# Kernel optimization log

Measured on AMD Instinct MI355X. Metric: run time of the kernel, lower is better.

## Reference

```python
import jax, jax.numpy as jnp
import numpy as np

# --- tkbn KbNufftAdjoint defaults for im_size=(128,128) ---
H, W = 128, 128          # im_size
GX, GY = 256, 256        # grid_size = 2 * im_size (default oversampling)
J = 6                    # numpoints (KB kernel width)
ALPHA = 2.34 * J         # tkbn default kb_alpha
I0_ALPHA = float(np.i0(ALPHA))


def _kb_ft_1d(om):
    # Fourier transform of order-0 Kaiser-Bessel kernel (Fessler), d=1.
    z = np.sqrt((np.pi * J * om) ** 2 - ALPHA ** 2 + 0j)
    return np.real(J * np.sinc(z / np.pi)) / np.i0(ALPHA)


def _apodization():
    # scaling coefficients: 1 / FT(kb) at centered image coords (tkbn compute_scaling_coefs)
    ax = 1.0 / _kb_ft_1d((np.arange(H) - (H - 1) / 2.0) / GX)
    ay = 1.0 / _kb_ft_1d((np.arange(W) - (W - 1) / 2.0) / GY)
    return jnp.asarray(np.outer(ax, ay), dtype=jnp.float32)  # [H, W]


def _kb_weights(gm, G):
    # gm: [K] fractional grid coords. Returns weights [K, J] and wrapped indices [K, J].
    base = jnp.floor(gm - J / 2.0)                       # [K]
    k = base[:, None] + jnp.arange(1, J + 1)[None, :]    # [K, J], offsets in (-J/2, J/2]
    u = gm[:, None] - k
    arg = 1.0 - (2.0 * u / J) ** 2
    w = jnp.where(arg > 0, jnp.i0(ALPHA * jnp.sqrt(jnp.maximum(arg, 1e-12))) / I0_ALPHA, 0.0)
    return w.astype(jnp.float32), jnp.mod(k, G).astype(jnp.int32)


def setup_inputs() -> dict:
    key = jax.random.key(0)
    k1, k2 = jax.random.split(key)
    values = jax.random.normal(k1, (8, 4, 32768), dtype=jnp.float32)
    coords = (jax.random.uniform(k2, (32768, 2), dtype=jnp.float32) * 2.0 - 1.0) * jnp.pi
    return {"values": values, "coords": coords}


def reference(values, coords):
    B, C, K = values.shape
    apod = _apodization()  # [H, W]

    # --- KB adjoint interpolation (gridding) onto oversampled grid ---
    gm_x = coords[:, 0] * (GX / (2.0 * jnp.pi))  # [K] fractional grid coords
    gm_y = coords[:, 1] * (GY / (2.0 * jnp.pi))
    wx, kx = _kb_weights(gm_x, GX)               # [K, J]
    wy, ky = _kb_weights(gm_y, GY)
    w = (wx[:, :, None] * wy[:, None, :]).reshape(K, J * J)                 # [K, 36]
    idx = (kx[:, :, None] * GY + ky[:, None, :]).reshape(K * J * J)        # [K*36]

    vals = values.astype(jnp.complex64)
    contrib = (vals[:, :, :, None] * w[None, None]).reshape(B, C, K * J * J)
    grid = jnp.zeros((B, C, GX * GY), dtype=jnp.complex64).at[:, :, idx].add(contrib)
    grid = grid.reshape(B, C, GX, GY)

    # --- true adjoint of unnormalized FFT: N * ifft, crop, apodize ---
    img = jnp.fft.ifft2(grid) * (GX * GY)
    img = img[..., :H, :W] * apod[None, None]    # [B, C, H, W] complex64

    # --- recon = |fftshift(fft2(img))| ; torch fftshift shifts ALL dims by default ---
    recon = jnp.abs(jnp.fft.fftshift(jnp.fft.fft2(img)))
    return recon
```

## Files before the change

### kernel.cpp

```cpp
#include <hip/hip_runtime.h>
#include <math.h>

#define NPTS 32768
#define CAPP 192
#define CAPC 57
#define SCALE ((float)(256.0 / (2.0 * M_PI)))

typedef __attribute__((ext_vector_type(8))) short short8b;
typedef __attribute__((ext_vector_type(4))) float f32x4;

static __device__ __forceinline__ unsigned short f2bf(float x) {
    unsigned u = __float_as_uint(x);
    return (unsigned short)((u + 0x7fffu + ((u >> 16) & 1u)) >> 16);
}

static __device__ __forceinline__ float bessel_i0f(float x) {
    float hx2 = 0.25f * x * x;
    float t = 1.0f, s = 1.0f;
#pragma unroll
    for (int m = 1; m <= 30; ++m) { t *= hx2 * (1.0f / ((float)m * (float)m)); s += t; }
    return s;
}

__global__ void k_zero(unsigned* __restrict__ tc) {
    tc[blockIdx.x * 256 + threadIdx.x] = 0u;
}

__global__ __launch_bounds__(256) void k_front(
        const float* __restrict__ coords, const float* __restrict__ values,
        unsigned short* __restrict__ Sfrag, float* __restrict__ wxy,
        unsigned* __restrict__ tileCount, unsigned* __restrict__ bins,
        float* __restrict__ vt) {
    __shared__ float tile[32][257];
    __shared__ float axf[128];
    __shared__ float2 sSh[256];
    int blk = blockIdx.x;
    int t = threadIdx.x;

    if (blk < 128) {
        int k = blk * 256 + t;
        const float inv_i0a = 1.0f / bessel_i0f(14.04f);
        float2 cv = *(const float2*)&coords[2 * k];
        float gmx = cv.x * SCALE;
        float gmy = cv.y * SCALE;
        float bxf = floorf(gmx - 3.0f), byf = floorf(gmy - 3.0f);
        float wl[12];
#pragma unroll
        for (int j = 0; j < 6; ++j) {
            float ux = gmx - (bxf + (float)(j + 1));
            float rx = ux * (1.0f / 3.0f);
            float argx = 1.0f - rx * rx;
            wl[j] = (argx > 0.0f) ? bessel_i0f(14.04f * sqrtf(argx)) * inv_i0a : 0.0f;
            float uy = gmy - (byf + (float)(j + 1));
            float ry = uy * (1.0f / 3.0f);
            float argy = 1.0f - ry * ry;
            wl[6 + j] = (argy > 0.0f) ? bessel_i0f(14.04f * sqrtf(argy)) * inv_i0a : 0.0f;
        }
        float4* wp = (float4*)&wxy[k * 12];
        wp[0] = *(const float4*)&wl[0];
        wp[1] = *(const float4*)&wl[4];
        wp[2] = *(const float4*)&wl[8];
        int x0 = (((int)bxf) + 1 + 512) & 255;
        int y0 = (((int)byf) + 1 + 512) & 255;
        int tx0 = x0 >> 3, tx1 = ((x0 + 5) & 255) >> 3;
        int ty0 = y0 >> 3, ty1 = ((y0 + 5) & 255) >> 3;
        int nx = (tx1 == tx0) ? 1 : 2;
        int ny = (ty1 == ty0) ? 1 : 2;
        int txs[2] = {tx0, tx1}, tys[2] = {ty0, ty1};
        for (int i = 0; i < nx; ++i)
            for (int j = 0; j < ny; ++j) {
                int tl = txs[i] * 32 + tys[j];
                unsigned ex = (unsigned)((x0 - 8 * txs[i] + 256) & 255);
                unsigned ey = (unsigned)((y0 - 8 * tys[j] + 256) & 255);
                unsigned pos = atomicAdd(&tileCount[tl * 16], 1u);
                if (pos < CAPP) bins[tl * CAPP + pos] = ((unsigned)k << 16) | (ex << 8) | ey;
            }
    } else {
        int kbase = (blk - 128) * 256;
        for (int img = 0; img < 32; ++img)
            tile[img][t] = values[img * NPTS + kbase + t];
        __syncthreads();
        int img = t & 31;
        int k0 = t >> 5;
        for (int r = 0; r < 32; ++r) {
            int kl = k0 + r * 8;
            vt[(kbase + kl) * 32 + img] = tile[img][kl];
        }
        int s = blk - 128;
        if (s < 8) {
            if (t < 128) {
                const float inv_i0a = 1.0f / bessel_i0f(14.04f);
                float om = ((float)t - 63.5f) * (1.0f / 256.0f);
                float pj = (float)M_PI * 6.0f * om;
                float tt = sqrtf(14.04f * 14.04f - pj * pj);
                float kbft = 6.0f * (sinhf(tt) / tt) * inv_i0a;
                axf[t] = 1.0f / kbft;
            }
            __syncthreads();
            float sw, cw;
            __sincosf((float)t * (float)(2.0 * M_PI / 256.0), &sw, &cw);
            float zr = 1.0f, zi = 0.0f, re = 0.0f, im = 0.0f;
            for (int x = 0; x < 128; ++x) {
                float a = axf[x];
                re = fmaf(a, zr, re);
                im = fmaf(a, zi, im);
                float nzr = zr * cw - zi * sw;
                zi = fmaf(zr, sw, zi * cw);
                zr = nzr;
            }
            sSh[t] = make_float2(re, im);
            __syncthreads();
            for (int idx = s * 4096 + t; idx < (s + 1) * 4096; idx += 256) {
                int i   = idx & 7;
                int ln  = (idx >> 3) & 63;
                int ks  = (idx >> 9) & 7;
                int tl  = idx >> 12;
                int si = (32 * ks + 8 * (ln >> 4) + i - 2 * (16 * tl + (ln & 15))) & 255;
                float2 sv = sSh[si];
                Sfrag[idx]         = f2bf(sv.x);
                Sfrag[32768 + idx] = f2bf(sv.y);
                Sfrag[65536 + idx] = f2bf(-sv.y);
            }
        }
    }
}

__global__ __launch_bounds__(256) void k_gather_tile(
        const float* __restrict__ wxy, const float* __restrict__ vt,
        const unsigned* __restrict__ tileCount, const unsigned* __restrict__ bins,
        unsigned short* __restrict__ Gt) {
    __shared__ unsigned cnt[64];
    __shared__ unsigned lists[64 * CAPC];
    __shared__ unsigned bsh[CAPP];
    __shared__ unsigned short gsh[64][40];
    int tile = blockIdx.x;
    int TX = tile >> 5, TY = tile & 31;
    int t = threadIdx.x;
    if (t < 64) cnt[t] = 0u;
    unsigned n = tileCount[tile * 16];
    if (n > CAPP) n = CAPP;
    for (int p = t; p < (int)n; p += 256) bsh[p] = bins[tile * CAPP + p];
    __syncthreads();
    int total = (int)n * 6;
    for (int task = t; task < total; task += 256) {
        int pi = task / 6;
        int jx = task - pi * 6;
        unsigned en = bsh[pi];
        int ex = (int)((en >> 8) & 255u);
        int ey = (int)(en & 255u);
        if (((ex + jx) & 255) < 8) {
            unsigned k = en >> 16;
            float wxv = wxy[k * 12 + jx];
            int lx = ((ex + jx) & 7) << 3;
            unsigned kq = k << 16;
            int jy0, jy1;
            if (ey <= 7) { jy0 = 0; jy1 = (7 - ey < 5) ? 7 - ey : 5; }
            else         { jy0 = 256 - ey; jy1 = 5; }
            for (int jy = jy0; jy <= jy1; ++jy) {
                float w = wxv * wxy[k * 12 + 6 + jy];
                unsigned q = (unsigned)(w * 65535.0f + 0.5f);
                if (q > 65535u) q = 65535u;
                int cl = lx | ((ey + jy) & 7);
                unsigned pos = atomicAdd(&cnt[cl], 1u);
                if (pos < CAPC) lists[cl * CAPC + pos] = kq | q;
            }
        }
    }
    __syncthreads();
    int c = t >> 2;
    int ib = (t & 3) * 8;
    unsigned nc = cnt[c];
    if (nc > CAPC) nc = CAPC;
    float acc0 = 0, acc1 = 0, acc2 = 0, acc3 = 0, acc4 = 0, acc5 = 0, acc6 = 0, acc7 = 0;
    for (unsigned e = 0; e < nc; ++e) {
        unsigned en = lists[c * CAPC + e];
        float w = (float)(en & 0xFFFFu) * (1.0f / 65535.0f);
        const float* vp = &vt[(en >> 16) * 32 + ib];
        float4 va = *(const float4*)vp;
        float4 vb = *(const float4*)(vp + 4);
        acc0 += w * va.x; acc1 += w * va.y; acc2 += w * va.z; acc3 += w * va.w;
        acc4 += w * vb.x; acc5 += w * vb.y; acc6 += w * vb.z; acc7 += w * vb.w;
    }
    {
        unsigned short* gp = &gsh[c][ib];
        gp[0] = f2bf(acc0); gp[1] = f2bf(acc1); gp[2] = f2bf(acc2); gp[3] = f2bf(acc3);
        gp[4] = f2bf(acc4); gp[5] = f2bf(acc5); gp[6] = f2bf(acc6); gp[7] = f2bf(acc7);
    }
    __syncthreads();
    {
        int img = t >> 3;
        int vr = t & 7;
        short8b row;
#pragma unroll
        for (int uu = 0; uu < 8; ++uu)
            row[uu] = (short)gsh[(uu << 3) | vr][img];
        *(short8b*)&Gt[img * 65536 + (((TY << 3) + vr) << 8) + (TX << 3)] = row;
    }
}

__global__ __launch_bounds__(512) void k_mmx(const unsigned short* __restrict__ Gt,
                                             const unsigned short* __restrict__ Sfrag,
                                             float* __restrict__ out) {
    __shared__ unsigned short T1[2][16][264];
    int t = threadIdx.x;
    int lane = t & 63;
    int w = t >> 6;
    int band = blockIdx.x;
    int img = blockIdx.y;
    int g4 = lane >> 4;
    int l15 = lane & 15;

    {
        int var = w >> 2;
        const unsigned short* sf = Sfrag + var * 32768 + band * 4096 + lane * 8;
        short8b a[8];
#pragma unroll
        for (int ks = 0; ks < 8; ++ks)
            a[ks] = *(const short8b*)(sf + ks * 512);
        const unsigned short* gimg = Gt + img * 65536 + 8 * g4;
#pragma unroll
        for (int j = 0; j < 4; ++j) {
            int vtile = (w & 3) + j * 4;
            int v0 = vtile * 16;
            const unsigned short* gb = gimg + (v0 + l15) * 256;
            f32x4 acc = {0.f, 0.f, 0.f, 0.f};
#pragma unroll
            for (int ks = 0; ks < 8; ++ks) {
                short8b b = *(const short8b*)(gb + ks * 32);
                acc = __builtin_amdgcn_mfma_f32_16x16x32_bf16(a[ks], b, acc, 0, 0, 0);
            }
            int vcol = v0 + l15;
#pragma unroll
            for (int r = 0; r < 4; ++r) {
                int p = g4 * 4 + r;
                T1[var][p][vcol ^ ((p & 7) << 3)] = f2bf(acc[r]);
            }
        }
    }
    __syncthreads();

    {
        int qt = w;
        const unsigned short* sfq = Sfrag + qt * 4096 + lane * 8;
        int swz = (l15 & 7) << 3;
        f32x4 accR = {0.f, 0.f, 0.f, 0.f}, accI = {0.f, 0.f, 0.f, 0.f};
#pragma unroll
        for (int ks = 0; ks < 8; ++ks) {
            int vidx = (32 * ks + 8 * g4) ^ swz;
            short8b aR = *(const short8b*)&T1[0][l15][vidx];
            short8b aI = *(const short8b*)&T1[1][l15][vidx];
            short8b bR = *(const short8b*)(sfq + ks * 512);
            short8b bI = *(const short8b*)(sfq + 32768 + ks * 512);
            short8b bN = *(const short8b*)(sfq + 65536 + ks * 512);
            accR = __builtin_amdgcn_mfma_f32_16x16x32_bf16(aR, bR, accR, 0, 0, 0);
            accR = __builtin_amdgcn_mfma_f32_16x16x32_bf16(aI, bN, accR, 0, 0, 0);
            accI = __builtin_amdgcn_mfma_f32_16x16x32_bf16(aR, bI, accI, 0, 0, 0);
            accI = __builtin_amdgcn_mfma_f32_16x16x32_bf16(aI, bR, accI, 0, 0, 0);
        }
        int q = qt * 16 + l15;
        int b_ = img >> 2, c_ = img & 3;
        int obase = ((b_ ^ 4) * 4 + (c_ ^ 2)) * 128;
#pragma unroll
        for (int r = 0; r < 4; ++r) {
            int p = band * 16 + g4 * 4 + r;
            float re = accR[r], im = accI[r];
            out[((obase + (p ^ 64)) << 7) + (q ^ 64)] = sqrtf(re * re + im * im);
        }
    }
}

extern "C" void kernel_launch(void* const* d_in, const int* in_sizes, int n_in,
                              void* d_out, int out_size, void* d_ws, size_t ws_size,
                              hipStream_t stream) {
    const float* values = (const float*)d_in[0];
    const float* coords = (const float*)d_in[1];

    char* ws = (char*)d_ws;
    unsigned short* Sfrag = (unsigned short*)(ws + 0);
    unsigned* tileCount   = (unsigned*)(ws + 196608);
    float*    wxy         = (float*)(ws + 262144);
    unsigned* bins        = (unsigned*)(ws + 1835008);
    unsigned short* Gt    = (unsigned short*)(ws + 2621440);
    float*    vt          = (float*)(ws + 6815744);

    k_zero<<<64, 256, 0, stream>>>(tileCount);
    k_front<<<256, 256, 0, stream>>>(coords, values, Sfrag, wxy, tileCount, bins, vt);
    k_gather_tile<<<1024, 256, 0, stream>>>(wxy, vt, tileCount, bins, Gt);
    k_mmx<<<dim3(8, 32), 512, 0, stream>>>(Gt, Sfrag, (float*)d_out);
}
```

Measured before the change: 50.43 us.

## Fuse all four kernels into one cooperative persistent kernel with grid syncs

Replaces the zero, front, gather and mmx launches with a single cooperative kernel of 256 blocks × 512 threads, separated by grid-wide syncs. Each block now handles four gather tiles, two per 256-thread half, using a shared-memory union. The aim is to remove three kernel launch gaps and the tail drain between stages. In exchange it adds grid-sync overhead and lowers parallelism in the gather stage, with 256 blocks instead of 1024.

```diff
diff --git a/kernel.cpp b/kernel.cpp
--- a/kernel.cpp
+++ b/kernel.cpp
@@ -1,5 +1,8 @@
 #include <hip/hip_runtime.h>
+#include <hip/hip_cooperative_groups.h>
 #include <math.h>
+
+namespace cg = cooperative_groups;
 
 #define NPTS 32768
 #define CAPP 192
@@ -22,23 +25,25 @@
     return s;
 }
 
-__global__ void k_zero(unsigned* __restrict__ tc) {
-    tc[blockIdx.x * 256 + threadIdx.x] = 0u;
-}
-
-__global__ __launch_bounds__(256) void k_front(
+__global__ __launch_bounds__(512) void k_mega(
         const float* __restrict__ coords, const float* __restrict__ values,
         unsigned short* __restrict__ Sfrag, float* __restrict__ wxy,
         unsigned* __restrict__ tileCount, unsigned* __restrict__ bins,
-        float* __restrict__ vt) {
-    __shared__ float tile[32][257];
-    __shared__ float axf[128];
-    __shared__ float2 sSh[256];
+        float* __restrict__ vt, unsigned short* __restrict__ Gt,
+        float* __restrict__ out) {
+    __shared__ __align__(16) char smem[41984];
+    cg::grid_group grid = cg::this_grid();
     int blk = blockIdx.x;
     int t = threadIdx.x;
 
-    if (blk < 128) {
-        int k = blk * 256 + t;
+    {
+        int gid = blk * 512 + t;
+        if (gid < 16384) tileCount[gid] = 0u;
+    }
+    grid.sync();
+
+    if (blk < 64) {
+        int k = blk * 512 + t;
         const float inv_i0a = 1.0f / bessel_i0f(14.04f);
         float2 cv = *(const float2*)&coords[2 * k];
         float gmx = cv.x * SCALE;
@@ -75,28 +80,32 @@
                 unsigned pos = atomicAdd(&tileCount[tl * 16], 1u);
                 if (pos < CAPP) bins[tl * CAPP + pos] = ((unsigned)k << 16) | (ex << 8) | ey;
             }
-    } else {
-        int kbase = (blk - 128) * 256;
-        for (int img = 0; img < 32; ++img)
-            tile[img][t] = values[img * NPTS + kbase + t];
+    } else if (blk < 192) {
+        float (*tile)[257] = (float(*)[257])smem;
+        int kbase = (blk - 64) * 256;
+        int col = t & 255;
+        for (int img = t >> 8; img < 32; img += 2)
+            tile[img][col] = values[img * NPTS + kbase + col];
         __syncthreads();
         int img = t & 31;
         int k0 = t >> 5;
-        for (int r = 0; r < 32; ++r) {
-            int kl = k0 + r * 8;
+        for (int r = 0; r < 16; ++r) {
+            int kl = k0 + r * 16;
             vt[(kbase + kl) * 32 + img] = tile[img][kl];
         }
-        int s = blk - 128;
-        if (s < 8) {
-            if (t < 128) {
-                const float inv_i0a = 1.0f / bessel_i0f(14.04f);
-                float om = ((float)t - 63.5f) * (1.0f / 256.0f);
-                float pj = (float)M_PI * 6.0f * om;
-                float tt = sqrtf(14.04f * 14.04f - pj * pj);
-                float kbft = 6.0f * (sinhf(tt) / tt) * inv_i0a;
-                axf[t] = 1.0f / kbft;
-            }
-            __syncthreads();
+    } else if (blk < 200) {
+        float* axf = (float*)smem;
+        float2* sSh = (float2*)(smem + 512);
+        if (t < 128) {
+            const float inv_i0a = 1.0f / bessel_i0f(14.04f);
+            float om = ((float)t - 63.5f) * (1.0f / 256.0f);
+            float pj = (float)M_PI * 6.0f * om;
+            float tt = sqrtf(14.04f * 14.04f - pj * pj);
+            float kbft = 6.0f * (sinhf(tt) / tt) * inv_i0a;
+            axf[t] = 1.0f / kbft;
+        }
+        __syncthreads();
+        if (t < 256) {
             float sw, cw;
             __sincosf((float)t * (float)(2.0 * M_PI / 256.0), &sw, &cw);
             float zr = 1.0f, zi = 0.0f, re = 0.0f, im = 0.0f;
@@ -109,162 +118,164 @@
                 zr = nzr;
             }
             sSh[t] = make_float2(re, im);
+        }
+        __syncthreads();
+        int s = blk - 192;
+        for (int idx = s * 4096 + t; idx < (s + 1) * 4096; idx += 512) {
+            int i   = idx & 7;
+            int ln  = (idx >> 3) & 63;
+            int ks  = (idx >> 9) & 7;
+            int tl  = idx >> 12;
+            int si = (32 * ks + 8 * (ln >> 4) + i - 2 * (16 * tl + (ln & 15))) & 255;
+            float2 sv = sSh[si];
+            Sfrag[idx]         = f2bf(sv.x);
+            Sfrag[32768 + idx] = f2bf(sv.y);
+            Sfrag[65536 + idx] = f2bf(-sv.y);
+        }
+    }
+    grid.sync();
+
+    {
+        int s = t >> 8;
+        int tt = t & 255;
+        char* base = smem + s * 20736;
+        unsigned* cnt = (unsigned*)base;
+        unsigned* lists = cnt + 64;
+        unsigned* bsh = lists + 64 * CAPC;
+        unsigned short (*gsh)[40] = (unsigned short(*)[40])(bsh + CAPP);
+        for (int ti = 0; ti < 2; ++ti) {
+            int tile = blk * 4 + s * 2 + ti;
+            int TX = tile >> 5, TY = tile & 31;
             __syncthreads();
-            for (int idx = s * 4096 + t; idx < (s + 1) * 4096; idx += 256) {
-                int i   = idx & 7;
-                int ln  = (idx >> 3) & 63;
-                int ks  = (idx >> 9) & 7;
-                int tl  = idx >> 12;
-                int si = (32 * ks + 8 * (ln >> 4) + i - 2 * (16 * tl + (ln & 15))) & 255;
-                float2 sv = sSh[si];
-                Sfrag[idx]         = f2bf(sv.x);
-                Sfrag[32768 + idx] = f2bf(sv.y);
-                Sfrag[65536 + idx] = f2bf(-sv.y);
+            if (tt < 64) cnt[tt] = 0u;
+            unsigned n = tileCount[tile * 16];
+            if (n > CAPP) n = CAPP;
+            for (int p = tt; p < (int)n; p += 256) bsh[p] = bins[tile * CAPP + p];
+            __syncthreads();
+            int total = (int)n * 6;
+            for (int task = tt; task < total; task += 256) {
+                int pi = task / 6;
+                int jx = task - pi * 6;
+                unsigned en = bsh[pi];
+                int ex = (int)((en >> 8) & 255u);
+                int ey = (int)(en & 255u);
+                if (((ex + jx) & 255) < 8) {
+                    unsigned k = en >> 16;
+                    float wxv = wxy[k * 12 + jx];
+                    int lx = ((ex + jx) & 7) << 3;
+                    unsigned kq = k << 16;
+                    int jy0, jy1;
+                    if (ey <= 7) { jy0 = 0; jy1 = (7 - ey < 5) ? 7 - ey : 5; }
+                    else         { jy0 = 256 - ey; jy1 = 5; }
+                    for (int jy = jy0; jy <= jy1; ++jy) {
+                        float w = wxv * wxy[k * 12 + 6 + jy];
+                        unsigned q = (unsigned)(w * 65535.0f + 0.5f);
+                        if (q > 65535u) q = 65535u;
+                        int cl = lx | ((ey + jy) & 7);
+                        unsigned pos = atomicAdd(&cnt[cl], 1u);
+                        if (pos < CAPC) lists[cl * CAPC + pos] = kq | q;
+                    }
+                }
+            }
+            __syncthreads();
+            int c = tt >> 2;
+            int ib = (tt & 3) * 8;
+            unsigned nc = cnt[c];
+            if (nc > CAPC) nc = CAPC;
+            float acc0 = 0, acc1 = 0, acc2 = 0, acc3 = 0, acc4 = 0, acc5 = 0, acc6 = 0, acc7 = 0;
+            for (unsigned e = 0; e < nc; ++e) {
+                unsigned en = lists[c * CAPC + e];
+                float w = (float)(en & 0xFFFFu) * (1.0f / 65535.0f);
+                const float* vp = &vt[(en >> 16) * 32 + ib];
+                float4 va = *(const float4*)vp;
+                float4 vb = *(const float4*)(vp + 4);
+                acc0 += w * va.x; acc1 += w * va.y; acc2 += w * va.z; acc3 += w * va.w;
+                acc4 += w * vb.x; acc5 += w * vb.y; acc6 += w * vb.z; acc7 += w * vb.w;
+            }
+            {
+                unsigned short* gp = &gsh[c][ib];
+                gp[0] = f2bf(acc0); gp[1] = f2bf(acc1); gp[2] = f2bf(acc2); gp[3] = f2bf(acc3);
+                gp[4] = f2bf(acc4); gp[5] = f2bf(acc5); gp[6] = f2bf(acc6); gp[7] = f2bf(acc7);
+            }
+            __syncthreads();
+            {
+                int img = tt >> 3;
+                int vr = tt & 7;
+                short8b row;
+#pragma unroll
+                for (int uu = 0; uu < 8; ++uu)
+                    row[uu] = (short)gsh[(uu << 3) | vr][img];
+                *(short8b*)&Gt[img * 65536 + (((TY << 3) + vr) << 8) + (TX << 3)] = row;
             }
         }
     }
-}
-
-__global__ __launch_bounds__(256) void k_gather_tile(
-        const float* __restrict__ wxy, const float* __restrict__ vt,
-        const unsigned* __restrict__ tileCount, const unsigned* __restrict__ bins,
-        unsigned short* __restrict__ Gt) {
-    __shared__ unsigned cnt[64];
-    __shared__ unsigned lists[64 * CAPC];
-    __shared__ unsigned bsh[CAPP];
-    __shared__ unsigned short gsh[64][40];
-    int tile = blockIdx.x;
-    int TX = tile >> 5, TY = tile & 31;
-    int t = threadIdx.x;
-    if (t < 64) cnt[t] = 0u;
-    unsigned n = tileCount[tile * 16];
-    if (n > CAPP) n = CAPP;
-    for (int p = t; p < (int)n; p += 256) bsh[p] = bins[tile * CAPP + p];
-    __syncthreads();
-    int total = (int)n * 6;
-    for (int task = t; task < total; task += 256) {
-        int pi = task / 6;
-        int jx = task - pi * 6;
-        unsigned en = bsh[pi];
-        int ex = (int)((en >> 8) & 255u);
-        int ey = (int)(en & 255u);
-        if (((ex + jx) & 255) < 8) {
-            unsigned k = en >> 16;
-            float wxv = wxy[k * 12 + jx];
-            int lx = ((ex + jx) & 7) << 3;
-            unsigned kq = k << 16;
-            int jy0, jy1;
-            if (ey <= 7) { jy0 = 0; jy1 = (7 - ey < 5) ? 7 - ey : 5; }
-            else         { jy0 = 256 - ey; jy1 = 5; }
-            for (int jy = jy0; jy <= jy1; ++jy) {
-                float w = wxv * wxy[k * 12 + 6 + jy];
-                unsigned q = (unsigned)(w * 65535.0f + 0.5f);
-                if (q > 65535u) q = 65535u;
-                int cl = lx | ((ey + jy) & 7);
-                unsigned pos = atomicAdd(&cnt[cl], 1u);
-                if (pos < CAPC) lists[cl * CAPC + pos] = kq | q;
-            }
-        }
-    }
-    __syncthreads();
-    int c = t >> 2;
-    int ib = (t & 3) * 8;
-    unsigned nc = cnt[c];
-    if (nc > CAPC) nc = CAPC;
-    float acc0 = 0, acc1 = 0, acc2 = 0, acc3 = 0, acc4 = 0, acc5 = 0, acc6 = 0, acc7 = 0;
-    for (unsigned e = 0; e < nc; ++e) {
-        unsigned en = lists[c * CAPC + e];
-        float w = (float)(en & 0xFFFFu) * (1.0f / 65535.0f);
-        const float* vp = &vt[(en >> 16) * 32 + ib];
-        float4 va = *(const float4*)vp;
-        float4 vb = *(const float4*)(vp + 4);
-        acc0 += w * va.x; acc1 += w * va.y; acc2 += w * va.z; acc3 += w * va.w;
-        acc4 += w * vb.x; acc5 += w * vb.y; acc6 += w * vb.z; acc7 += w * vb.w;
-    }
+    grid.sync();
+
     {
-        unsigned short* gp = &gsh[c][ib];
-        gp[0] = f2bf(acc0); gp[1] = f2bf(acc1); gp[2] = f2bf(acc2); gp[3] = f2bf(acc3);
-        gp[4] = f2bf(acc4); gp[5] = f2bf(acc5); gp[6] = f2bf(acc6); gp[7] = f2bf(acc7);
-    }
-    __syncthreads();
-    {
-        int img = t >> 3;
-        int vr = t & 7;
-        short8b row;
-#pragma unroll
-        for (int uu = 0; uu < 8; ++uu)
-            row[uu] = (short)gsh[(uu << 3) | vr][img];
-        *(short8b*)&Gt[img * 65536 + (((TY << 3) + vr) << 8) + (TX << 3)] = row;
-    }
-}
-
-__global__ __launch_bounds__(512) void k_mmx(const unsigned short* __restrict__ Gt,
-                                             const unsigned short* __restrict__ Sfrag,
-                                             float* __restrict__ out) {
-    __shared__ unsigned short T1[2][16][264];
-    int t = threadIdx.x;
-    int lane = t & 63;
-    int w = t >> 6;
-    int band = blockIdx.x;
-    int img = blockIdx.y;
-    int g4 = lane >> 4;
-    int l15 = lane & 15;
-
-    {
-        int var = w >> 2;
-        const unsigned short* sf = Sfrag + var * 32768 + band * 4096 + lane * 8;
-        short8b a[8];
-#pragma unroll
-        for (int ks = 0; ks < 8; ++ks)
-            a[ks] = *(const short8b*)(sf + ks * 512);
-        const unsigned short* gimg = Gt + img * 65536 + 8 * g4;
-#pragma unroll
-        for (int j = 0; j < 4; ++j) {
-            int vtile = (w & 3) + j * 4;
-            int v0 = vtile * 16;
-            const unsigned short* gb = gimg + (v0 + l15) * 256;
-            f32x4 acc = {0.f, 0.f, 0.f, 0.f};
+        unsigned short* T1 = (unsigned short*)smem;
+        int band = blk >> 5;
+        int img = blk & 31;
+        int lane = t & 63;
+        int w = t >> 6;
+        int g4 = lane >> 4;
+        int l15 = lane & 15;
+
+        {
+            int var = w >> 2;
+            const unsigned short* sf = Sfrag + var * 32768 + band * 4096 + lane * 8;
+            short8b a[8];
+#pragma unroll
+            for (int ks = 0; ks < 8; ++ks)
+                a[ks] = *(const short8b*)(sf + ks * 512);
+            const unsigned short* gimg = Gt + img * 65536 + 8 * g4;
+#pragma unroll
+            for (int j = 0; j < 4; ++j) {
+                int vtile = (w & 3) + j * 4;
+                int v0 = vtile * 16;
+                const unsigned short* gb = gimg + (v0 + l15) * 256;
+                f32x4 acc = {0.f, 0.f, 0.f, 0.f};
+#pragma unroll
+                for (int ks = 0; ks < 8; ++ks) {
+                    short8b b = *(const short8b*)(gb + ks * 32);
+                    acc = __builtin_amdgcn_mfma_f32_16x16x32_bf16(a[ks], b, acc, 0, 0, 0);
+                }
+                int vcol = v0 + l15;
+#pragma unroll
+                for (int r = 0; r < 4; ++r) {
+                    int p = g4 * 4 + r;
+                    T1[var * 4224 + p * 264 + (vcol ^ ((p & 7) << 3))] = f2bf(acc[r]);
+                }
+            }
+        }
+        __syncthreads();
+
+        {
+            int qt = w;
+            const unsigned short* sfq = Sfrag + qt * 4096 + lane * 8;
+            int swz = (l15 & 7) << 3;
+            f32x4 accR = {0.f, 0.f, 0.f, 0.f}, accI = {0.f, 0.f, 0.f, 0.f};
 #pragma unroll
             for (int ks = 0; ks < 8; ++ks) {
-                short8b b = *(const short8b*)(gb + ks * 32);
-                acc = __builtin_amdgcn_mfma_f32_16x16x32_bf16(a[ks], b, acc, 0, 0, 0);
-            }
-            int vcol = v0 + l15;
+                int vidx = (32 * ks + 8 * g4) ^ swz;
+                short8b aR = *(const short8b*)&T1[0 * 4224 + l15 * 264 + vidx];
+                short8b aI = *(const short8b*)&T1[1 * 4224 + l15 * 264 + vidx];
+                short8b bR = *(const short8b*)(sfq + ks * 512);
+                short8b bI = *(const short8b*)(sfq + 32768 + ks * 512);
+                short8b bN = *(const short8b*)(sfq + 65536 + ks * 512);
+                accR = __builtin_amdgcn_mfma_f32_16x16x32_bf16(aR, bR, accR, 0, 0, 0);
+                accR = __builtin_amdgcn_mfma_f32_16x16x32_bf16(aI, bN, accR, 0, 0, 0);
+                accI = __builtin_amdgcn_mfma_f32_16x16x32_bf16(aR, bI, accI, 0, 0, 0);
+                accI = __builtin_amdgcn_mfma_f32_16x16x32_bf16(aI, bR, accI, 0, 0, 0);
+            }
+            int q = qt * 16 + l15;
+            int b_ = img >> 2, c_ = img & 3;
+            int obase = ((b_ ^ 4) * 4 + (c_ ^ 2)) * 128;
 #pragma unroll
             for (int r = 0; r < 4; ++r) {
-                int p = g4 * 4 + r;
-                T1[var][p][vcol ^ ((p & 7) << 3)] = f2bf(acc[r]);
-            }
-        }
-    }
-    __syncthreads();
-
-    {
-        int qt = w;
-        const unsigned short* sfq = Sfrag + qt * 4096 + lane * 8;
-        int swz = (l15 & 7) << 3;
-        f32x4 accR = {0.f, 0.f, 0.f, 0.f}, accI = {0.f, 0.f, 0.f, 0.f};
-#pragma unroll
-        for (int ks = 0; ks < 8; ++ks) {
-            int vidx = (32 * ks + 8 * g4) ^ swz;
-            short8b aR = *(const short8b*)&T1[0][l15][vidx];
-            short8b aI = *(const short8b*)&T1[1][l15][vidx];
-            short8b bR = *(const short8b*)(sfq + ks * 512);
-            short8b bI = *(const short8b*)(sfq + 32768 + ks * 512);
-            short8b bN = *(const short8b*)(sfq + 65536 + ks * 512);
-            accR = __builtin_amdgcn_mfma_f32_16x16x32_bf16(aR, bR, accR, 0, 0, 0);
-            accR = __builtin_amdgcn_mfma_f32_16x16x32_bf16(aI, bN, accR, 0, 0, 0);
-            accI = __builtin_amdgcn_mfma_f32_16x16x32_bf16(aR, bI, accI, 0, 0, 0);
-            accI = __builtin_amdgcn_mfma_f32_16x16x32_bf16(aI, bR, accI, 0, 0, 0);
-        }
-        int q = qt * 16 + l15;
-        int b_ = img >> 2, c_ = img & 3;
-        int obase = ((b_ ^ 4) * 4 + (c_ ^ 2)) * 128;
-#pragma unroll
-        for (int r = 0; r < 4; ++r) {
-            int p = band * 16 + g4 * 4 + r;
-            float re = accR[r], im = accI[r];
-            out[((obase + (p ^ 64)) << 7) + (q ^ 64)] = sqrtf(re * re + im * im);
+                int p = band * 16 + g4 * 4 + r;
+                float re = accR[r], im = accI[r];
+                out[((obase + (p ^ 64)) << 7) + (q ^ 64)] = sqrtf(re * re + im * im);
+            }
         }
     }
 }
@@ -282,9 +293,9 @@
     unsigned* bins        = (unsigned*)(ws + 1835008);
     unsigned short* Gt    = (unsigned short*)(ws + 2621440);
     float*    vt          = (float*)(ws + 6815744);
-
-    k_zero<<<64, 256, 0, stream>>>(tileCount);
-    k_front<<<256, 256, 0, stream>>>(coords, values, Sfrag, wxy, tileCount, bins, vt);
-    k_gather_tile<<<1024, 256, 0, stream>>>(wxy, vt, tileCount, bins, Gt);
-    k_mmx<<<dim3(8, 32), 512, 0, stream>>>(Gt, Sfrag, (float*)d_out);
+    float*    out         = (float*)d_out;
+
+    void* args[] = {(void*)&coords, (void*)&values, (void*)&Sfrag, (void*)&wxy,
+                    (void*)&tileCount, (void*)&bins, (void*)&vt, (void*)&Gt, (void*)&out};
+    hipLaunchCooperativeKernel((void*)k_mega, dim3(256), dim3(512), args, 0, stream);
 }
```

Measured after the change: 137.6 us. 173% more time.

## Bin points per block in shared memory and drop the zeroing kernel

Applied to the files above, without the earlier changes.

The binning step now counts points per tile with shared-memory atomics inside each front block and writes them into fixed per-(tile, block) slots of 16 entries, storing packed byte counts. This removes the global atomics and the separate zeroing launch. The gather kernel compacts the 128 per-block slots into its shared list with a local atomic. The matmul grid is also flattened to one dimension with a different band/image block ordering. The risk is silently dropping points if more than 16 land in one tile from one block, and the gather now performs a scattered 128-way read.

```diff
diff --git a/kernel.cpp b/kernel.cpp
--- a/kernel.cpp
+++ b/kernel.cpp
@@ -4,6 +4,7 @@
 #define NPTS 32768
 #define CAPP 192
 #define CAPC 57
+#define SLOT 16
 #define SCALE ((float)(256.0 / (2.0 * M_PI)))
 
 typedef __attribute__((ext_vector_type(8))) short short8b;
@@ -22,15 +23,12 @@
     return s;
 }
 
-__global__ void k_zero(unsigned* __restrict__ tc) {
-    tc[blockIdx.x * 256 + threadIdx.x] = 0u;
-}
-
 __global__ __launch_bounds__(256) void k_front(
         const float* __restrict__ coords, const float* __restrict__ values,
         unsigned short* __restrict__ Sfrag, float* __restrict__ wxy,
-        unsigned* __restrict__ tileCount, unsigned* __restrict__ bins,
+        unsigned* __restrict__ cnts32, unsigned* __restrict__ bins2,
         float* __restrict__ vt) {
+    __shared__ unsigned cnt[1024];
     __shared__ float tile[32][257];
     __shared__ float axf[128];
     __shared__ float2 sSh[256];
@@ -38,6 +36,8 @@
     int t = threadIdx.x;
 
     if (blk < 128) {
+        for (int i = t; i < 1024; i += 256) cnt[i] = 0u;
+        __syncthreads();
         int k = blk * 256 + t;
         const float inv_i0a = 1.0f / bessel_i0f(14.04f);
         float2 cv = *(const float2*)&coords[2 * k];
@@ -72,9 +72,16 @@
                 int tl = txs[i] * 32 + tys[j];
                 unsigned ex = (unsigned)((x0 - 8 * txs[i] + 256) & 255);
                 unsigned ey = (unsigned)((y0 - 8 * tys[j] + 256) & 255);
-                unsigned pos = atomicAdd(&tileCount[tl * 16], 1u);
-                if (pos < CAPP) bins[tl * CAPP + pos] = ((unsigned)k << 16) | (ex << 8) | ey;
-            }
+                unsigned pos = atomicAdd(&cnt[tl], 1u);
+                if (pos < SLOT)
+                    bins2[(tl * 128 + blk) * SLOT + pos] = ((unsigned)k << 16) | (ex << 8) | ey;
+            }
+        __syncthreads();
+        unsigned c0 = cnt[4 * t],     c1 = cnt[4 * t + 1];
+        unsigned c2 = cnt[4 * t + 2], c3 = cnt[4 * t + 3];
+        c0 = c0 > SLOT ? SLOT : c0;  c1 = c1 > SLOT ? SLOT : c1;
+        c2 = c2 > SLOT ? SLOT : c2;  c3 = c3 > SLOT ? SLOT : c3;
+        cnts32[blk * 256 + t] = c0 | (c1 << 8) | (c2 << 16) | (c3 << 24);
     } else {
         int kbase = (blk - 128) * 256;
         for (int img = 0; img < 32; ++img)
@@ -127,8 +134,9 @@
 
 __global__ __launch_bounds__(256) void k_gather_tile(
         const float* __restrict__ wxy, const float* __restrict__ vt,
-        const unsigned* __restrict__ tileCount, const unsigned* __restrict__ bins,
+        const unsigned* __restrict__ cnts32, const unsigned* __restrict__ bins2,
         unsigned short* __restrict__ Gt) {
+    __shared__ unsigned np;
     __shared__ unsigned cnt[64];
     __shared__ unsigned lists[64 * CAPC];
     __shared__ unsigned bsh[CAPP];
@@ -136,11 +144,22 @@
     int tile = blockIdx.x;
     int TX = tile >> 5, TY = tile & 31;
     int t = threadIdx.x;
+    if (t == 0) np = 0u;
     if (t < 64) cnt[t] = 0u;
-    unsigned n = tileCount[tile * 16];
+    __syncthreads();
+    if (t < 128) {
+        unsigned word = cnts32[t * 256 + (tile >> 2)];
+        unsigned cb = (word >> ((tile & 3) * 8)) & 0xFFu;
+        if (cb) {
+            unsigned pos = atomicAdd(&np, cb);
+            const unsigned* src = &bins2[(tile * 128 + t) * SLOT];
+            for (unsigned e = 0; e < cb; ++e)
+                if (pos + e < CAPP) bsh[pos + e] = src[e];
+        }
+    }
+    __syncthreads();
+    unsigned n = np;
     if (n > CAPP) n = CAPP;
-    for (int p = t; p < (int)n; p += 256) bsh[p] = bins[tile * CAPP + p];
-    __syncthreads();
     int total = (int)n * 6;
     for (int task = t; task < total; task += 256) {
         int pi = task / 6;
@@ -202,11 +221,12 @@
                                              const unsigned short* __restrict__ Sfrag,
                                              float* __restrict__ out) {
     __shared__ unsigned short T1[2][16][264];
+    int blk = blockIdx.x;
+    int band = blk >> 5;
+    int img = blk & 31;
     int t = threadIdx.x;
     int lane = t & 63;
     int w = t >> 6;
-    int band = blockIdx.x;
-    int img = blockIdx.y;
     int g4 = lane >> 4;
     int l15 = lane & 15;
 
@@ -277,14 +297,13 @@
 
     char* ws = (char*)d_ws;
     unsigned short* Sfrag = (unsigned short*)(ws + 0);
-    unsigned* tileCount   = (unsigned*)(ws + 196608);
     float*    wxy         = (float*)(ws + 262144);
-    unsigned* bins        = (unsigned*)(ws + 1835008);
-    unsigned short* Gt    = (unsigned short*)(ws + 2621440);
-    float*    vt          = (float*)(ws + 6815744);
-
-    k_zero<<<64, 256, 0, stream>>>(tileCount);
-    k_front<<<256, 256, 0, stream>>>(coords, values, Sfrag, wxy, tileCount, bins, vt);
-    k_gather_tile<<<1024, 256, 0, stream>>>(wxy, vt, tileCount, bins, Gt);
-    k_mmx<<<dim3(8, 32), 512, 0, stream>>>(Gt, Sfrag, (float*)d_out);
-}
+    unsigned* cnts32      = (unsigned*)(ws + 1835008);
+    unsigned* bins2       = (unsigned*)(ws + 1966080);
+    unsigned short* Gt    = (unsigned short*)(ws + 10354688);
+    float*    vt          = (float*)(ws + 14548992);
+
+    k_front<<<256, 256, 0, stream>>>(coords, values, Sfrag, wxy, cnts32, bins2, vt);
+    k_gather_tile<<<1024, 256, 0, stream>>>(wxy, vt, cnts32, bins2, Gt);
+    k_mmx<<<256, 512, 0, stream>>>(Gt, Sfrag, (float*)d_out);
+}
```

New measurement: 47.50 us. 1.06x faster.
